# Kernel tuning notes

Measured on AMD Instinct MI355X. Metric: run time of the kernel, lower is better.

The kernel has to match this reference:

```python
import jax, jax.numpy as jnp
import numpy as np

NUM_OBJECTS = 6          # self.NUM_OBJECTS
SCORE_THRESH = 1e-4      # self.score_tresh
NMS_THRESHS = jnp.asarray(np.arange(0.001, 1.0, 0.1), dtype=jnp.float32)  # 10 thresholds
K_CAND = 1024            # fixed-shape cap on (proposal,class) candidates per image
CLASS_OFFSET = 4096.0    # > max image coord; batched_nms per-class offset trick


def _iou_matrix(b):
    # b: [K,4] xyxy -> [K,K] IoU
    x1, y1, x2, y2 = b[:, 0], b[:, 1], b[:, 2], b[:, 3]
    area = (x2 - x1) * (y2 - y1)
    iw = jnp.clip(jnp.minimum(x2[:, None], x2[None, :]) - jnp.maximum(x1[:, None], x1[None, :]), 0.0)
    ih = jnp.clip(jnp.minimum(y2[:, None], y2[None, :]) - jnp.maximum(y1[:, None], y1[None, :]), 0.0)
    inter = iw * ih
    union = area[:, None] + area[None, :] - inter
    return jnp.where(union > 0, inter / union, 0.0)


def _greedy_nms(iou, valid, thresh):
    # candidates are pre-sorted by descending score; sequential greedy suppression
    K = valid.shape[0]
    ar = jnp.arange(K)
    def body(i, keep):
        sup = keep[i] & (iou[i] > thresh) & (ar > i)
        return keep & ~sup
    return jax.lax.fori_loop(0, K, body, valid)


def _per_image(logits, boxes, feats, hw):
    # logits [N,81], boxes [N,80,4], feats [N,2048], hw [2] (h,w)
    C = boxes.shape[1]
    probs = jax.nn.softmax(logits, axis=-1)[:, :C]          # drop background class
    h = hw[0].astype(boxes.dtype)
    w = hw[1].astype(boxes.dtype)
    b = jnp.stack([jnp.clip(boxes[..., 0], 0.0, w),         # clip to image
                   jnp.clip(boxes[..., 1], 0.0, h),
                   jnp.clip(boxes[..., 2], 0.0, w),
                   jnp.clip(boxes[..., 3], 0.0, h)], axis=-1)
    scores = probs.reshape(-1)                              # [N*C]
    vals, idx = jax.lax.top_k(jnp.where(scores > SCORE_THRESH, scores, -1.0), K_CAND)
    cand_valid = vals > SCORE_THRESH
    cb = b.reshape(-1, 4)[idx]                              # [K,4]
    cls = (idx % C).astype(boxes.dtype)
    prop = idx // C                                         # proposal row index
    iou = _iou_matrix(cb + cls[:, None] * CLASS_OFFSET)     # per-class NMS via offsets
    keeps = jax.vmap(lambda t: _greedy_nms(iou, cand_valid, t))(NMS_THRESHS)  # [T,K]
    counts = keeps.sum(axis=1)
    # torch loop: break at first (smallest) thresh yielding len(ids)==6, i.e. >=6 kept
    ok = counts >= NUM_OBJECTS
    t_sel = jnp.where(jnp.any(ok), jnp.argmax(ok), NMS_THRESHS.shape[0] - 1)
    keep = keeps[t_sel]
    _, top = jax.lax.top_k(jnp.where(keep, vals, -jnp.inf), NUM_OBJECTS)
    ids = prop[top]                                         # [6]
    return feats[ids].T                                     # [2048, 6] (permute(1,0))


def _forward(cls_logits, boxes, feature_pooled, image_hw):
    return jax.vmap(_per_image)(cls_logits, boxes, feature_pooled, image_hw)  # [B,2048,6]


def setup_inputs() -> dict:
    key = jax.random.key(0)
    k1, k2, k3, k4, k5 = jax.random.split(key, 5)
    B, N, C, D = 8, 1000, 80, 2048
    cls_logits = jax.random.normal(k1, (B, N, C + 1), dtype=jnp.float32)
    ctr = jax.random.uniform(k2, (B, N, C, 2), minval=0.0, maxval=800.0)
    sz = jax.random.uniform(k3, (B, N, C, 2), minval=8.0, maxval=200.0)
    boxes = jnp.concatenate([ctr - sz * 0.5, ctr + sz * 0.5], axis=-1).astype(jnp.float32)
    feature_pooled = jax.random.normal(k4, (B, N, D), dtype=jnp.float32)
    image_hw = jax.random.randint(k5, (B, 2), 600, 800, dtype=jnp.int32)
    return {"cls_logits": cls_logits, "boxes": boxes,
            "feature_pooled": feature_pooled, "image_hw": image_hw}


def reference(cls_logits, boxes, feature_pooled, image_hw):
    return _forward(cls_logits, boxes, feature_pooled, image_hw)
```

## Files before the change

### kernel.cpp

```cpp
#include <hip/hip_runtime.h>
#include <cmath>
#include <cstdint>

#define NB 8
#define NPROP 1000
#define NCLS 80
#define NLOG 81
#define KCAND 1024
#define NTH 10
#define DFEAT 2048
#define NOBJ 6
#define NSCORE (NPROP*NCLS)
#define HBLK 8
#define HCHUNK (NSCORE/HBLK)
#define PCHUNK (NPROP/HBLK)

constexpr size_t OFF_SCORES = 0;
constexpr size_t SZ_SCORES  = (size_t)NB * NSCORE * 4;
constexpr size_t OFF_LISTA  = OFF_SCORES + SZ_SCORES;
constexpr size_t SZ_LISTA   = (size_t)NB * 20 * KCAND * 8;
constexpr size_t OFF_H1     = OFF_LISTA;
constexpr size_t OFF_H2     = OFF_H1 + (size_t)NB * HBLK * 2048 * 4;
constexpr size_t OFF_PIV    = OFF_H2 + (size_t)NB * HBLK * 2048 * 4;
constexpr size_t OFF_CBUF   = OFF_PIV + (size_t)NB * 8 * 4;
constexpr size_t OFF_CANDK  = OFF_LISTA + SZ_LISTA;
constexpr size_t SZ_CANDK   = (size_t)NB * KCAND * 8;
constexpr size_t OFF_CX1    = OFF_CANDK + SZ_CANDK;
constexpr size_t SZ_CARR    = (size_t)NB * KCAND * 4;
constexpr size_t OFF_CY1    = OFF_CX1 + SZ_CARR;
constexpr size_t OFF_CX2    = OFF_CY1 + SZ_CARR;
constexpr size_t OFF_CY2    = OFF_CX2 + SZ_CARR;
constexpr size_t OFF_CAREA  = OFF_CY2 + SZ_CARR;
constexpr size_t OFF_CPROP  = OFF_CAREA + SZ_CARR;
constexpr size_t OFF_VALIDW = OFF_CPROP + SZ_CARR;
constexpr size_t SZ_VALIDW  = (size_t)NB * 16 * 8;
constexpr size_t OFF_MASKS  = OFF_VALIDW + SZ_VALIDW;
constexpr size_t SZ_MASKS   = (size_t)NTH * NB * KCAND * 16 * 8;
constexpr size_t OFF_KEEPS  = OFF_MASKS + SZ_MASKS;
constexpr size_t SZ_KEEPS   = (size_t)NB * NTH * 16 * 8;
constexpr size_t OFF_COUNTS = OFF_KEEPS + SZ_KEEPS;
constexpr size_t SZ_COUNTS  = (size_t)NB * NTH * 4;
constexpr size_t OFF_CCLS   = OFF_COUNTS + SZ_COUNTS;
constexpr size_t SZ_CCLS    = (size_t)NB * KCAND * 4;

#define TSTRIDE ((size_t)NB * 16 * 1024)

__device__ __forceinline__ float nms_th(int t) {
    return (float)(0.001 + 0.1 * (double)t);
}

__device__ __forceinline__ unsigned score_vkey(float v) {
    float vv = (v > 1e-4f) ? v : -1.0f;
    unsigned bits = __float_as_uint(vv);
    unsigned u = (bits & 0x80000000u) ? ~bits : (bits | 0x80000000u);
    return ~u;
}

__global__ void k_memz(ulonglong2* __restrict__ p, int n) {
    int g = blockIdx.x * blockDim.x + threadIdx.x;
    if (g < n) p[g] = ulonglong2{0ULL, 0ULL};
}

__global__ __launch_bounds__(1024) void k_softhist(const float* __restrict__ logits,
                                                   float* __restrict__ scores,
                                                   unsigned* __restrict__ hist1) {
    __shared__ unsigned hh[2048];
    int img = blockIdx.x >> 3, blk = blockIdx.x & 7;
    int tid = threadIdx.x, wid = tid >> 6, lane = tid & 63;
    hh[tid] = 0; hh[tid + 1024] = 0;
    __syncthreads();
    for (int p = wid; p < PCHUNK; p += 16) {
        int prop = blk * PCHUNK + p;
        const float* L = logits + ((size_t)img * NPROP + prop) * NLOG;
        float l0 = L[lane];
        float l1 = (lane < 17) ? L[64 + lane] : -INFINITY;
        float m = fmaxf(l0, l1);
        #pragma unroll
        for (int o = 32; o > 0; o >>= 1) m = fmaxf(m, __shfl_xor(m, o, 64));
        float e0 = expf(l0 - m);
        float e1 = (lane < 17) ? expf(l1 - m) : 0.f;
        float s = e0 + e1;
        #pragma unroll
        for (int o = 32; o > 0; o >>= 1) s += __shfl_xor(s, o, 64);
        float* op = scores + ((size_t)img * NPROP + prop) * NCLS;
        float p0 = e0 / s;
        op[lane] = p0;
        atomicAdd(&hh[score_vkey(p0) >> 21], 1u);
        if (lane < 16) {
            float p1 = e1 / s;
            op[64 + lane] = p1;
            atomicAdd(&hh[score_vkey(p1) >> 21], 1u);
        }
    }
    __syncthreads();
    unsigned* outp = hist1 + ((size_t)img * HBLK + blk) * 2048;
    outp[tid] = hh[tid];
    outp[tid + 1024] = hh[tid + 1024];
}

__device__ __forceinline__ void pivot_scan(const unsigned* __restrict__ h8, unsigned K,
                                           int* __restrict__ out_b, int* __restrict__ out_rem) {
    __shared__ unsigned wsum[16];
    int tid = threadIdx.x;
    unsigned a = 0, b = 0;
    #pragma unroll
    for (int s = 0; s < HBLK; ++s) {
        a += h8[s * 2048 + 2 * tid];
        b += h8[s * 2048 + 2 * tid + 1];
    }
    unsigned p = a + b;
    unsigned x = p;
    #pragma unroll
    for (int d = 1; d < 64; d <<= 1) {
        unsigned y = __shfl_up(x, (unsigned)d, 64);
        if ((tid & 63) >= d) x += y;
    }
    if ((tid & 63) == 63) wsum[tid >> 6] = x;
    __syncthreads();
    if (tid < 16) {
        unsigned w = wsum[tid];
        #pragma unroll
        for (int d = 1; d < 16; d <<= 1) {
            unsigned y = __shfl_up(w, (unsigned)d, 64);
            if (tid >= d) w += y;
        }
        wsum[tid] = w;
    }
    __syncthreads();
    unsigned wex = (tid >= 64) ? wsum[(tid >> 6) - 1] : 0u;
    unsigned incl = x + wex;
    unsigned E = incl - p;
    if (E < K && E + a >= K)              { *out_b = 2 * tid;     *out_rem = (int)(K - E); }
    else if (E + a < K && E + a + b >= K) { *out_b = 2 * tid + 1; *out_rem = (int)(K - (E + a)); }
}

__global__ __launch_bounds__(1024) void k_hist2p(const float* __restrict__ scores,
                                                 const unsigned* __restrict__ hist1,
                                                 unsigned* __restrict__ hist2,
                                                 int* __restrict__ piv) {
    __shared__ unsigned hh[2048];
    __shared__ int sb, sr;
    int img = blockIdx.x >> 3, blk = blockIdx.x & 7;
    int tid = threadIdx.x;
    hh[tid] = 0; hh[tid + 1024] = 0;
    pivot_scan(hist1 + (size_t)img * HBLK * 2048, KCAND, &sb, &sr);
    __syncthreads();
    unsigned b1 = (unsigned)sb;
    const float* sc = scores + (size_t)img * NSCORE + (size_t)blk * HCHUNK;
    for (int e = tid; e < HCHUNK; e += 1024) {
        unsigned vk = score_vkey(sc[e]);
        if ((vk >> 21) == b1) atomicAdd(&hh[(vk >> 10) & 2047u], 1u);
    }
    __syncthreads();
    unsigned* outp = hist2 + ((size_t)img * HBLK + blk) * 2048;
    outp[tid] = hh[tid];
    outp[tid + 1024] = hh[tid + 1024];
    if (blk == 0 && tid == 0) {
        piv[img * 8 + 0] = sb;
        piv[img * 8 + 1] = sr;
        piv[img * 8 + 3] = 0;
    }
}

__global__ __launch_bounds__(1024) void k_gatherp(const float* __restrict__ scores,
                                                  const unsigned* __restrict__ hist2,
                                                  int* __restrict__ piv,
                                                  unsigned long long* __restrict__ cbuf) {
    __shared__ int sb2, sr2;
    __shared__ unsigned lcnt, gbase;
    int img = blockIdx.x >> 3, blk = blockIdx.x & 7;
    int tid = threadIdx.x;
    if (tid == 0) lcnt = 0;
    unsigned K2 = (unsigned)piv[img * 8 + 1];
    pivot_scan(hist2 + (size_t)img * HBLK * 2048, K2, &sb2, &sr2);
    __syncthreads();
    unsigned T22 = ((unsigned)piv[img * 8 + 0] << 11) | (unsigned)sb2;
    const float* sc = scores + (size_t)img * NSCORE + (size_t)blk * HCHUNK;
    unsigned long long sel[(HCHUNK + 1023) / 1024];
    int ns = 0;
    for (int e = tid; e < HCHUNK; e += 1024) {
        unsigned vk = score_vkey(sc[e]);
        if ((vk >> 10) <= T22)
            sel[ns++] = ((unsigned long long)vk << 32) | (unsigned)(blk * HCHUNK + e);
    }
    unsigned lp = atomicAdd(&lcnt, (unsigned)ns);
    __syncthreads();
    if (tid == 0) gbase = atomicAdd((unsigned*)&piv[img * 8 + 3], lcnt);
    __syncthreads();
    unsigned long long* ob = cbuf + (size_t)img * 2048;
    for (int i = 0; i < ns; ++i) {
        unsigned pos = gbase + lp + (unsigned)i;
        if (pos < 2048) ob[pos] = sel[i];
    }
}

__global__ __launch_bounds__(256) void k_rankcand(const unsigned long long* __restrict__ cbuf,
                                                  const int* __restrict__ piv,
                                                  const float* __restrict__ boxes,
                                                  const int* __restrict__ hw,
                                                  float* __restrict__ cx1, float* __restrict__ cy1,
                                                  float* __restrict__ cx2, float* __restrict__ cy2,
                                                  float* __restrict__ car, int* __restrict__ cprop,
                                                  int* __restrict__ ccls,
                                                  unsigned long long* __restrict__ validw) {
    __shared__ unsigned long long keys[2048];
    int img = blockIdx.x >> 3, sl = blockIdx.x & 7;
    int tid = threadIdx.x;
    int cnt = piv[img * 8 + 3]; if (cnt > 2048) cnt = 2048;
    const unsigned long long* ib = cbuf + (size_t)img * 2048;
    #pragma unroll
    for (int k = 0; k < 8; ++k) {
        int t = k * 256 + tid;
        keys[t] = (t < cnt) ? ib[t] : ~0ULL;
    }
    __syncthreads();
    unsigned long long a = keys[sl * 256 + tid];
    int r = 0;
    #pragma unroll 8
    for (int j = 0; j < cnt; ++j) r += (keys[j] < a) ? 1 : 0;
    if (r < KCAND) {
        unsigned u   = ~(unsigned)(a >> 32);
        unsigned idx = (unsigned)a;
        const unsigned uth = __float_as_uint(1e-4f) | 0x80000000u;
        bool valid = u > uth;
        int prop = (int)(idx / NCLS);
        int cls  = (int)(idx - (unsigned)prop * NCLS);
        const float4 bx = *(const float4*)(boxes + ((((size_t)img * NPROP + prop) * NCLS + cls) << 2));
        float h = (float)hw[img * 2 + 0];
        float w = (float)hw[img * 2 + 1];
        float x1 = fminf(fmaxf(bx.x, 0.f), w);
        float y1 = fminf(fmaxf(bx.y, 0.f), h);
        float x2 = fminf(fmaxf(bx.z, 0.f), w);
        float y2 = fminf(fmaxf(bx.w, 0.f), h);
        float offc = __fmul_rn((float)cls, 4096.0f);
        x1 = __fadd_rn(x1, offc); y1 = __fadd_rn(y1, offc);
        x2 = __fadd_rn(x2, offc); y2 = __fadd_rn(y2, offc);
        float area = __fmul_rn(__fsub_rn(x2, x1), __fsub_rn(y2, y1));
        int o = img * KCAND + r;
        cx1[o] = x1; cy1[o] = y1; cx2[o] = x2; cy2[o] = y2;
        car[o] = area; cprop[o] = prop; ccls[o] = cls;
        if (valid) atomicOr(&validw[img * 16 + (r >> 6)], 1ULL << (r & 63));
    }
}

__global__ void k_masks(const float* __restrict__ cx1, const float* __restrict__ cy1,
                        const float* __restrict__ cx2, const float* __restrict__ cy2,
                        const float* __restrict__ car, const int* __restrict__ ccls,
                        unsigned long long* __restrict__ masks) {
    int gw   = (blockIdx.x * blockDim.x + threadIdx.x) >> 6;
    int lane = threadIdx.x & 63;
    if (gw >= NB * KCAND) return;
    int bimg = gw >> 10;
    int i    = gw & (KCAND - 1);
    int cb   = bimg * KCAND;
    int   ci  = ccls[cb + i];
    float xi1 = cx1[cb + i], yi1 = cy1[cb + i];
    float xi2 = cx2[cb + i], yi2 = cy2[cb + i], ai = car[cb + i];
    int cmax = i >> 6;
    for (int c = 0; c <= cmax; ++c) {
        int j = c * 64 + lane;
        bool jlt = j < i;
        int cj = ccls[cb + j];
        if (__ballot(jlt && (cj == ci)) == 0ULL) continue;
        float xj1 = cx1[cb + j], yj1 = cy1[cb + j];
        float xj2 = cx2[cb + j], yj2 = cy2[cb + j], aj = car[cb + j];
        float iw = fmaxf(__fsub_rn(fminf(xi2, xj2), fmaxf(xi1, xj1)), 0.f);
        float ih = fmaxf(__fsub_rn(fminf(yi2, yj2), fmaxf(yi1, yj1)), 0.f);
        float inter = __fmul_rn(iw, ih);
        if (__ballot(jlt && (inter > 0.f)) == 0ULL) continue;
        float uni = __fsub_rn(__fadd_rn(ai, aj), inter);
        float iou = (uni > 0.f) ? __fdiv_rn(inter, uni) : 0.f;
        unsigned long long bl[NTH];
        #pragma unroll
        for (int t = 0; t < NTH; ++t) bl[t] = __ballot(jlt && (iou > nms_th(t)));
        unsigned long long myv = 0;
        #pragma unroll
        for (int t = 0; t < NTH; ++t) myv = (lane == t) ? bl[t] : myv;
        if (lane < NTH)
            masks[(size_t)lane * TSTRIDE + (((size_t)(bimg * 16 + c)) << 10) + i] = myv;
    }
}

__global__ __launch_bounds__(1024) void k_scan(const unsigned long long* __restrict__ masks,
                                               const unsigned long long* __restrict__ validw,
                                               unsigned long long* __restrict__ keeps,
                                               int* __restrict__ counts) {
    __shared__ unsigned long long kp[16];
    __shared__ int changed[2];
    int bt   = blockIdx.x;
    int bimg = bt / NTH, t = bt % NTH;
    int tid  = threadIdx.x;
    int w    = tid >> 6;
    int lane = tid & 63;
    const unsigned long long* mb = masks + (size_t)t * TSTRIDE + ((size_t)(bimg * 16) << 10);
    unsigned long long row[16];
    #pragma unroll
    for (int c = 0; c < 16; ++c)
        row[c] = (c <= w) ? mb[((size_t)c << 10) + tid] : 0ULL;
    unsigned long long vw = validw[bimg * 16 + w];
    bool valid = (vw >> lane) & 1ULL;
    if (tid < 16) kp[tid] = validw[bimg * 16 + tid];
    if (tid < 2) changed[tid] = 0;
    __syncthreads();
    for (int iter = 0; iter < KCAND + 2; ++iter) {
        unsigned long long s = 0;
        #pragma unroll
        for (int c = 0; c < 16; ++c) s |= row[c] & kp[c];
        bool nk = valid && (s == 0);
        unsigned long long bal = __ballot(nk);
        bool diff = (lane == 0) && (bal != kp[w]);
        __syncthreads();
        if (diff) { kp[w] = bal; changed[iter & 1] = 1; }
        if (tid == 0) changed[(iter + 1) & 1] = 0;
        __syncthreads();
        if (!changed[iter & 1]) break;
    }
    if (tid < 16) keeps[((size_t)bimg * NTH + t) * 16 + tid] = kp[tid];
    if (tid < 64) {
        int c = (lane < 16) ? __popcll(kp[lane]) : 0;
        #pragma unroll
        for (int o = 32; o > 0; o >>= 1) c += __shfl_xor(c, o, 64);
        if (lane == 0) counts[bimg * NTH + t] = c;
    }
}

__global__ __launch_bounds__(256) void k_selfeat(const int* __restrict__ counts,
                                                 const unsigned long long* __restrict__ keeps,
                                                 const int* __restrict__ cprop,
                                                 const float* __restrict__ feats,
                                                 float* __restrict__ outp) {
    __shared__ int scnt[NTH];
    __shared__ unsigned long long skw[16];
    __shared__ int stsel;
    __shared__ int sids[NOBJ];
    int img = blockIdx.x >> 3;
    int tid = threadIdx.x;
    if (tid < NTH) scnt[tid] = counts[img * NTH + tid];
    __syncthreads();
    if (tid == 0) {
        int tsel = NTH - 1;
        for (int t = 0; t < NTH; ++t) if (scnt[t] >= NOBJ) { tsel = t; break; }
        stsel = tsel;
    }
    __syncthreads();
    if (tid < 16) skw[tid] = keeps[((size_t)img * NTH + stsel) * 16 + tid];
    __syncthreads();
    if (tid == 0) {
        int got = 0;
        for (int k = 0; k < 16 && got < NOBJ; ++k) {
            unsigned long long x = skw[k];
            while (x && got < NOBJ) {
                int b = __builtin_ctzll(x);
                sids[got++] = cprop[img * KCAND + k * 64 + b];
                x &= x - 1;
            }
        }
        for (int k = 0; k < 16 && got < NOBJ; ++k) {
            unsigned long long x = ~skw[k];
            while (x && got < NOBJ) {
                int b = __builtin_ctzll(x);
                sids[got++] = cprop[img * KCAND + k * 64 + b];
                x &= x - 1;
            }
        }
    }
    __syncthreads();
    int d = (blockIdx.x & 7) * 256 + tid;
    const float* fb = feats + (size_t)img * NPROP * DFEAT;
    float* ob = outp + ((size_t)img * DFEAT + d) * NOBJ;
    #pragma unroll
    for (int s = 0; s < NOBJ; ++s)
        ob[s] = fb[(size_t)sids[s] * DFEAT + d];
}

extern "C" void kernel_launch(void* const* d_in, const int* in_sizes, int n_in,
                              void* d_out, int out_size, void* d_ws, size_t ws_size,
                              hipStream_t stream) {
    const float* logits = (const float*)d_in[0];
    const float* boxes  = (const float*)d_in[1];
    const float* feats  = (const float*)d_in[2];
    const int*   hw     = (const int*)d_in[3];
    float* outp = (float*)d_out;

    char* ws = (char*)d_ws;
    float*              scores = (float*)(ws + OFF_SCORES);
    unsigned*           hist1  = (unsigned*)(ws + OFF_H1);
    unsigned*           hist2  = (unsigned*)(ws + OFF_H2);
    int*                piv    = (int*)(ws + OFF_PIV);
    unsigned long long* cbuf   = (unsigned long long*)(ws + OFF_CBUF);
    float* cx1 = (float*)(ws + OFF_CX1);
    float* cy1 = (float*)(ws + OFF_CY1);
    float* cx2 = (float*)(ws + OFF_CX2);
    float* cy2 = (float*)(ws + OFF_CY2);
    float* car = (float*)(ws + OFF_CAREA);
    int*   cprop = (int*)(ws + OFF_CPROP);
    int*   ccls  = (int*)(ws + OFF_CCLS);
    unsigned long long* validw = (unsigned long long*)(ws + OFF_VALIDW);
    unsigned long long* masks  = (unsigned long long*)(ws + OFF_MASKS);
    unsigned long long* keeps  = (unsigned long long*)(ws + OFF_KEEPS);
    int* counts = (int*)(ws + OFF_COUNTS);

    const int mz_n = (int)((SZ_VALIDW + SZ_MASKS) / 16);
    k_memz<<<(mz_n + 255) / 256, 256, 0, stream>>>((ulonglong2*)(ws + OFF_VALIDW), mz_n);
    k_softhist<<<NB * HBLK, 1024, 0, stream>>>(logits, scores, hist1);
    k_hist2p<<<NB * HBLK, 1024, 0, stream>>>(scores, hist1, hist2, piv);
    k_gatherp<<<NB * HBLK, 1024, 0, stream>>>(scores, hist2, piv, cbuf);
    k_rankcand<<<NB * HBLK, 256, 0, stream>>>(cbuf, piv, boxes, hw,
                                              cx1, cy1, cx2, cy2, car, cprop, ccls, validw);
    k_masks<<<(NB * KCAND) / 4, 256, 0, stream>>>(cx1, cy1, cx2, cy2, car, ccls, masks);
    k_scan<<<NB * NTH, 1024, 0, stream>>>(masks, validw, keeps, counts);
    k_selfeat<<<NB * HBLK, 256, 0, stream>>>(counts, keeps, cprop, feats, outp);
}
```

Baseline: 169.4 us.

## Fuse the NMS pipeline into one cooperative kernel with grid syncs

Replaces the chain of eight kernel launches with a single cooperative mega-kernel of 256 blocks that separates the stages with grid.sync(). It also reorganises the work split: 32 blocks per image for softmax and histograms, and a warp-per-row mask build that skips chunks with no same-class or overlapping pairs. The aim is to remove launch gaps and tail idling between the small stages. In exchange, several stages now run on only a few blocks (rank on 32, scan on 80) while the rest wait at the barrier. If the cooperative launch fails, the old multi-kernel path still runs.

```diff
diff --git a/kernel.cpp b/kernel.cpp
--- a/kernel.cpp
+++ b/kernel.cpp
@@ -1,6 +1,9 @@
 #include <hip/hip_runtime.h>
+#include <hip/hip_cooperative_groups.h>
 #include <cmath>
 #include <cstdint>
+
+namespace cg = cooperative_groups;
 
 #define NB 8
 #define NPROP 1000
@@ -55,6 +58,332 @@
     unsigned u = (bits & 0x80000000u) ? ~bits : (bits | 0x80000000u);
     return ~u;
 }
+
+
+__device__ __forceinline__ void pivot512(const unsigned* __restrict__ h, unsigned K,
+                                         int* __restrict__ out_b, int* __restrict__ out_rem) {
+    __shared__ unsigned pwsum[8];
+    int tid = threadIdx.x, lane = tid & 63, wv = tid >> 6;
+    unsigned c0 = h[4 * tid + 0], c1 = h[4 * tid + 1];
+    unsigned c2 = h[4 * tid + 2], c3 = h[4 * tid + 3];
+    unsigned p = c0 + c1 + c2 + c3;
+    unsigned x = p;
+    #pragma unroll
+    for (int d = 1; d < 64; d <<= 1) {
+        unsigned y = __shfl_up(x, (unsigned)d, 64);
+        if (lane >= d) x += y;
+    }
+    if (lane == 63) pwsum[wv] = x;
+    __syncthreads();
+    if (tid < 8) {
+        unsigned w = pwsum[tid];
+        #pragma unroll
+        for (int d = 1; d < 8; d <<= 1) {
+            unsigned y = __shfl_up(w, (unsigned)d, 64);
+            if (tid >= d) w += y;
+        }
+        pwsum[tid] = w;
+    }
+    __syncthreads();
+    unsigned wex = wv ? pwsum[wv - 1] : 0u;
+    unsigned e0 = x + wex - p;
+    unsigned e1 = e0 + c0, e2 = e1 + c1, e3 = e2 + c2, e4 = e3 + c3;
+    if      (e0 < K && e1 >= K) { *out_b = 4 * tid + 0; *out_rem = (int)(K - e0); }
+    else if (e1 < K && e2 >= K) { *out_b = 4 * tid + 1; *out_rem = (int)(K - e1); }
+    else if (e2 < K && e3 >= K) { *out_b = 4 * tid + 2; *out_rem = (int)(K - e2); }
+    else if (e3 < K && e4 >= K) { *out_b = 4 * tid + 3; *out_rem = (int)(K - e3); }
+    __syncthreads();
+}
+
+__global__ __launch_bounds__(512, 2) void k_mega(
+        const float* __restrict__ logits, const float* __restrict__ boxes,
+        const float* __restrict__ feats, const int* __restrict__ hw,
+        float* __restrict__ outp,
+        float* __restrict__ scores, unsigned* __restrict__ gh1, unsigned* __restrict__ gh2,
+        int* __restrict__ cnt, unsigned long long* __restrict__ cbuf,
+        float* __restrict__ cx1, float* __restrict__ cy1,
+        float* __restrict__ cx2, float* __restrict__ cy2,
+        float* __restrict__ car, int* __restrict__ cprop, int* __restrict__ ccls,
+        unsigned long long* __restrict__ validw,
+        unsigned long long* __restrict__ masks,
+        unsigned long long* __restrict__ keeps, int* __restrict__ counts) {
+    cg::grid_group grid = cg::this_grid();
+    __shared__ union {
+        unsigned hist[2048];
+        unsigned long long keys[2048];
+        struct { int scnt[NTH]; unsigned long long skw[16]; int stsel; int sids[NOBJ]; } sel;
+    } sm;
+    __shared__ unsigned long long kp[16];
+    __shared__ int ichg[2];
+    __shared__ int sb1, sr1, sb2, sr2;
+    __shared__ unsigned lcnt, gbase;
+
+    const int blk = blockIdx.x;
+    const int tid = threadIdx.x;
+    const int wv  = tid >> 6, lane = tid & 63;
+    const int img = blk >> 5;
+    const int sl  = blk & 31;
+    const int pbeg = sl * 32;
+    const int pend = (pbeg + 32 < NPROP) ? (pbeg + 32) : NPROP;
+
+    {
+        int g = blk * 512 + tid;
+        if (g < NB * 2048) { gh1[g] = 0; gh2[g] = 0; }
+        if (g < NB) cnt[g] = 0;
+        if (g < NB * 16) validw[g] = 0ULL;
+    }
+    grid.sync();
+
+    {
+        #pragma unroll
+        for (int k = 0; k < 4; ++k) sm.hist[tid + k * 512] = 0;
+        __syncthreads();
+        for (int p = pbeg + wv; p < pend; p += 8) {
+            const float* L = logits + ((size_t)img * NPROP + p) * NLOG;
+            float l0 = L[lane];
+            float l1 = (lane < 17) ? L[64 + lane] : -INFINITY;
+            float m = fmaxf(l0, l1);
+            #pragma unroll
+            for (int o = 32; o > 0; o >>= 1) m = fmaxf(m, __shfl_xor(m, o, 64));
+            float e0 = expf(l0 - m);
+            float e1 = (lane < 17) ? expf(l1 - m) : 0.f;
+            float s = e0 + e1;
+            #pragma unroll
+            for (int o = 32; o > 0; o >>= 1) s += __shfl_xor(s, o, 64);
+            float* op = scores + ((size_t)img * NPROP + p) * NCLS;
+            float p0 = e0 / s;
+            op[lane] = p0;
+            atomicAdd(&sm.hist[score_vkey(p0) >> 21], 1u);
+            if (lane < 16) {
+                float p1 = e1 / s;
+                op[64 + lane] = p1;
+                atomicAdd(&sm.hist[score_vkey(p1) >> 21], 1u);
+            }
+        }
+        __syncthreads();
+        #pragma unroll
+        for (int k = 0; k < 4; ++k) {
+            unsigned v = sm.hist[tid + k * 512];
+            if (v) atomicAdd(&gh1[img * 2048 + tid + k * 512], v);
+        }
+    }
+    grid.sync();
+
+    {
+        pivot512(gh1 + (size_t)img * 2048, KCAND, &sb1, &sr1);
+        unsigned b1 = (unsigned)sb1;
+        #pragma unroll
+        for (int k = 0; k < 4; ++k) sm.hist[tid + k * 512] = 0;
+        __syncthreads();
+        const float* sc = scores + (size_t)img * NSCORE;
+        int ebeg = pbeg * NCLS, eend = pend * NCLS;
+        for (int e = ebeg + tid; e < eend; e += 512) {
+            unsigned vk = score_vkey(sc[e]);
+            if ((vk >> 21) == b1) atomicAdd(&sm.hist[(vk >> 10) & 2047u], 1u);
+        }
+        __syncthreads();
+        #pragma unroll
+        for (int k = 0; k < 4; ++k) {
+            unsigned v = sm.hist[tid + k * 512];
+            if (v) atomicAdd(&gh2[img * 2048 + tid + k * 512], v);
+        }
+    }
+    grid.sync();
+
+    {
+        pivot512(gh1 + (size_t)img * 2048, KCAND, &sb1, &sr1);
+        pivot512(gh2 + (size_t)img * 2048, (unsigned)sr1, &sb2, &sr2);
+        if (tid == 0) lcnt = 0;
+        __syncthreads();
+        unsigned T22 = ((unsigned)sb1 << 11) | (unsigned)sb2;
+        const float* sc = scores + (size_t)img * NSCORE;
+        int ebeg = pbeg * NCLS, eend = pend * NCLS;
+        unsigned long long selb[6];
+        int ns = 0;
+        for (int e = ebeg + tid; e < eend; e += 512) {
+            unsigned vk = score_vkey(sc[e]);
+            if ((vk >> 10) <= T22)
+                selb[ns++] = ((unsigned long long)vk << 32) | (unsigned)e;
+        }
+        unsigned lp = atomicAdd(&lcnt, (unsigned)ns);
+        __syncthreads();
+        if (tid == 0) gbase = atomicAdd((unsigned*)&cnt[img], lcnt);
+        __syncthreads();
+        unsigned long long* ob = cbuf + (size_t)img * 2048;
+        for (int i = 0; i < ns; ++i) {
+            unsigned pos = gbase + lp + (unsigned)i;
+            if (pos < 2048) ob[pos] = selb[i];
+        }
+    }
+    grid.sync();
+
+    if (sl < 4) {
+        int c = cnt[img]; if (c > 2048) c = 2048;
+        const unsigned long long* ib = cbuf + (size_t)img * 2048;
+        #pragma unroll
+        for (int k = 0; k < 4; ++k) {
+            int t = k * 512 + tid;
+            sm.keys[t] = (t < c) ? ib[t] : ~0ULL;
+        }
+        __syncthreads();
+        int my = sl * 512 + tid;
+        unsigned long long a = sm.keys[my];
+        int r = 0;
+        #pragma unroll 8
+        for (int j = 0; j < c; ++j) r += (sm.keys[j] < a) ? 1 : 0;
+        if (my < c && r < KCAND) {
+            unsigned u   = ~(unsigned)(a >> 32);
+            unsigned idx = (unsigned)a;
+            const unsigned uth = __float_as_uint(1e-4f) | 0x80000000u;
+            bool valid = u > uth;
+            int prop = (int)(idx / NCLS);
+            int cls  = (int)(idx - (unsigned)prop * NCLS);
+            const float4 bx = *(const float4*)(boxes + ((((size_t)img * NPROP + prop) * NCLS + cls) << 2));
+            float h = (float)hw[img * 2 + 0];
+            float w = (float)hw[img * 2 + 1];
+            float x1 = fminf(fmaxf(bx.x, 0.f), w);
+            float y1 = fminf(fmaxf(bx.y, 0.f), h);
+            float x2 = fminf(fmaxf(bx.z, 0.f), w);
+            float y2 = fminf(fmaxf(bx.w, 0.f), h);
+            float offc = __fmul_rn((float)cls, 4096.0f);
+            x1 = __fadd_rn(x1, offc); y1 = __fadd_rn(y1, offc);
+            x2 = __fadd_rn(x2, offc); y2 = __fadd_rn(y2, offc);
+            float area = __fmul_rn(__fsub_rn(x2, x1), __fsub_rn(y2, y1));
+            int o = img * KCAND + r;
+            cx1[o] = x1; cy1[o] = y1; cx2[o] = x2; cy2[o] = y2;
+            car[o] = area; cprop[o] = prop; ccls[o] = cls;
+            if (valid) atomicOr(&validw[img * 16 + (r >> 6)], 1ULL << (r & 63));
+        }
+    }
+    grid.sync();
+
+    {
+        int w = blk * 8 + wv;
+        for (int k = 0; k < 4; ++k) {
+            int rowg = w + 2048 * k;
+            int im = rowg >> 10;
+            int i  = rowg & 1023;
+            int cb = im * KCAND;
+            int   ci  = ccls[cb + i];
+            float xi1 = cx1[cb + i], yi1 = cy1[cb + i];
+            float xi2 = cx2[cb + i], yi2 = cy2[cb + i], ai = car[cb + i];
+            int cmax = i >> 6;
+            for (int c = 0; c <= cmax; ++c) {
+                int j = c * 64 + lane;
+                bool jlt = j < i;
+                unsigned long long bl[NTH];
+                #pragma unroll
+                for (int t = 0; t < NTH; ++t) bl[t] = 0ULL;
+                int cj = ccls[cb + j];
+                if (__ballot(jlt && (cj == ci)) != 0ULL) {
+                    float xj1 = cx1[cb + j], yj1 = cy1[cb + j];
+                    float xj2 = cx2[cb + j], yj2 = cy2[cb + j], aj = car[cb + j];
+                    float iw = fmaxf(__fsub_rn(fminf(xi2, xj2), fmaxf(xi1, xj1)), 0.f);
+                    float ih = fmaxf(__fsub_rn(fminf(yi2, yj2), fmaxf(yi1, yj1)), 0.f);
+                    float inter = __fmul_rn(iw, ih);
+                    if (__ballot(jlt && (inter > 0.f)) != 0ULL) {
+                        float uni = __fsub_rn(__fadd_rn(ai, aj), inter);
+                        float iou = (uni > 0.f) ? __fdiv_rn(inter, uni) : 0.f;
+                        #pragma unroll
+                        for (int t = 0; t < NTH; ++t) bl[t] = __ballot(jlt && (iou > nms_th(t)));
+                    }
+                }
+                unsigned long long myv = 0;
+                #pragma unroll
+                for (int t = 0; t < NTH; ++t) myv = (lane == t) ? bl[t] : myv;
+                if (lane < NTH)
+                    masks[(size_t)lane * TSTRIDE + (((size_t)(im * 16 + c)) << 10) + i] = myv;
+            }
+        }
+    }
+    grid.sync();
+
+    if (blk < NB * NTH) {
+        int im = blk / NTH, t = blk % NTH;
+        const unsigned long long* mb = masks + (size_t)t * TSTRIDE + ((size_t)(im * 16) << 10);
+        int iA = tid, iB = tid + 512;
+        int cA = iA >> 6;
+        int cB = iB >> 6;
+        unsigned long long rowA[8], rowB[16];
+        #pragma unroll
+        for (int c = 0; c < 8; ++c)  rowA[c] = (c <= cA) ? mb[((size_t)c << 10) + iA] : 0ULL;
+        #pragma unroll
+        for (int c = 0; c < 16; ++c) rowB[c] = (c <= cB) ? mb[((size_t)c << 10) + iB] : 0ULL;
+        bool vA = (validw[im * 16 + cA] >> (iA & 63)) & 1ULL;
+        bool vB = (validw[im * 16 + cB] >> (iB & 63)) & 1ULL;
+        if (tid < 16) kp[tid] = validw[im * 16 + tid];
+        if (tid < 2) ichg[tid] = 0;
+        __syncthreads();
+        for (int iter = 0; iter < KCAND + 2; ++iter) {
+            unsigned long long sA = 0, sB = 0;
+            #pragma unroll
+            for (int c = 0; c < 8; ++c)  sA |= rowA[c] & kp[c];
+            #pragma unroll
+            for (int c = 0; c < 16; ++c) sB |= rowB[c] & kp[c];
+            bool nkA = vA && (sA == 0);
+            bool nkB = vB && (sB == 0);
+            unsigned long long balA = __ballot(nkA);
+            unsigned long long balB = __ballot(nkB);
+            bool dA = (lane == 0) && (balA != kp[wv]);
+            bool dB = (lane == 0) && (balB != kp[wv + 8]);
+            __syncthreads();
+            if (dA) { kp[wv] = balA; ichg[iter & 1] = 1; }
+            if (dB) { kp[wv + 8] = balB; ichg[iter & 1] = 1; }
+            if (tid == 0) ichg[(iter + 1) & 1] = 0;
+            __syncthreads();
+            if (!ichg[iter & 1]) break;
+        }
+        if (tid < 16) keeps[((size_t)im * NTH + t) * 16 + tid] = kp[tid];
+        if (tid < 64) {
+            int c = (lane < 16) ? __popcll(kp[lane]) : 0;
+            #pragma unroll
+            for (int o = 32; o > 0; o >>= 1) c += __shfl_xor(c, o, 64);
+            if (lane == 0) counts[im * NTH + t] = c;
+        }
+    }
+    grid.sync();
+
+    if (blk < NB * 4) {
+        int im = blk >> 2;
+        if (tid < NTH) sm.sel.scnt[tid] = counts[im * NTH + tid];
+        __syncthreads();
+        if (tid == 0) {
+            int tsel = NTH - 1;
+            for (int t = 0; t < NTH; ++t) if (sm.sel.scnt[t] >= NOBJ) { tsel = t; break; }
+            sm.sel.stsel = tsel;
+        }
+        __syncthreads();
+        if (tid < 16) sm.sel.skw[tid] = keeps[((size_t)im * NTH + sm.sel.stsel) * 16 + tid];
+        __syncthreads();
+        if (tid == 0) {
+            int got = 0;
+            for (int k = 0; k < 16 && got < NOBJ; ++k) {
+                unsigned long long x = sm.sel.skw[k];
+                while (x && got < NOBJ) {
+                    int b = __builtin_ctzll(x);
+                    sm.sel.sids[got++] = cprop[im * KCAND + k * 64 + b];
+                    x &= x - 1;
+                }
+            }
+            for (int k = 0; k < 16 && got < NOBJ; ++k) {
+                unsigned long long x = ~sm.sel.skw[k];
+                while (x && got < NOBJ) {
+                    int b = __builtin_ctzll(x);
+                    sm.sel.sids[got++] = cprop[im * KCAND + k * 64 + b];
+                    x &= x - 1;
+                }
+            }
+        }
+        __syncthreads();
+        int d = (blk & 3) * 512 + tid;
+        const float* fb = feats + (size_t)im * NPROP * DFEAT;
+        float* ob = outp + ((size_t)im * DFEAT + d) * NOBJ;
+        #pragma unroll
+        for (int s = 0; s < NOBJ; ++s)
+            ob[s] = fb[(size_t)sm.sel.sids[s] * DFEAT + d];
+    }
+}
+
 
 __global__ void k_memz(ulonglong2* __restrict__ p, int n) {
     int g = blockIdx.x * blockDim.x + threadIdx.x;
@@ -400,6 +729,21 @@
     unsigned long long* keeps  = (unsigned long long*)(ws + OFF_KEEPS);
     int* counts = (int*)(ws + OFF_COUNTS);
 
+    {
+        unsigned* gh1 = hist1;
+        unsigned* gh2 = hist2;
+        int*      cnt = piv;
+        void* args[] = { (void*)&logits, (void*)&boxes, (void*)&feats, (void*)&hw, (void*)&outp,
+                         (void*)&scores, (void*)&gh1, (void*)&gh2, (void*)&cnt, (void*)&cbuf,
+                         (void*)&cx1, (void*)&cy1, (void*)&cx2, (void*)&cy2, (void*)&car,
+                         (void*)&cprop, (void*)&ccls, (void*)&validw,
+                         (void*)&masks, (void*)&keeps, (void*)&counts };
+        hipError_t e = hipLaunchCooperativeKernel((const void*)k_mega, dim3(256), dim3(512),
+                                                  args, 0, stream);
+        if (e == hipSuccess) return;
+        (void)hipGetLastError();
+    }
+
     const int mz_n = (int)((SZ_VALIDW + SZ_MASKS) / 16);
     k_memz<<<(mz_n + 255) / 256, 256, 0, stream>>>((ulonglong2*)(ws + OFF_VALIDW), mz_n);
     k_softhist<<<NB * HBLK, 1024, 0, stream>>>(logits, scores, hist1);
```

New measurement: 352.3 us. 108% more time.

## Replace global IoU masks and scan with per-class wavefront NMS

Applied to the files above, without the earlier changes.

Candidates are bucketed by class during ranking, and NMS for each (image, class) pair runs inside a single wavefront using shuffles and ballot-based fixed-point iteration across all thresholds. This removes the large mask buffer, its zeroing kernel, the mask kernel and the block-wide scan kernel, since the class offset means different classes never overlap. Zeroing of small buffers is folded into the gather kernel. The risk is the per-class cap of 64: a class with more than 64 candidates would silently drop entries.

```diff
diff --git a/kernel.cpp b/kernel.cpp
--- a/kernel.cpp
+++ b/kernel.cpp
@@ -14,6 +14,7 @@
 #define HBLK 8
 #define HCHUNK (NSCORE/HBLK)
 #define PCHUNK (NPROP/HBLK)
+#define CCAP 64
 
 constexpr size_t OFF_SCORES = 0;
 constexpr size_t SZ_SCORES  = (size_t)NB * NSCORE * 4;
@@ -34,16 +35,10 @@
 constexpr size_t OFF_CPROP  = OFF_CAREA + SZ_CARR;
 constexpr size_t OFF_VALIDW = OFF_CPROP + SZ_CARR;
 constexpr size_t SZ_VALIDW  = (size_t)NB * 16 * 8;
-constexpr size_t OFF_MASKS  = OFF_VALIDW + SZ_VALIDW;
-constexpr size_t SZ_MASKS   = (size_t)NTH * NB * KCAND * 16 * 8;
-constexpr size_t OFF_KEEPS  = OFF_MASKS + SZ_MASKS;
+constexpr size_t OFF_CCNT   = OFF_VALIDW + SZ_VALIDW;
+constexpr size_t OFF_CLIST  = OFF_CCNT + (size_t)NB * NCLS * 4;
+constexpr size_t OFF_KEEPS  = OFF_CLIST + (size_t)NB * NCLS * CCAP * 4;
 constexpr size_t SZ_KEEPS   = (size_t)NB * NTH * 16 * 8;
-constexpr size_t OFF_COUNTS = OFF_KEEPS + SZ_KEEPS;
-constexpr size_t SZ_COUNTS  = (size_t)NB * NTH * 4;
-constexpr size_t OFF_CCLS   = OFF_COUNTS + SZ_COUNTS;
-constexpr size_t SZ_CCLS    = (size_t)NB * KCAND * 4;
-
-#define TSTRIDE ((size_t)NB * 16 * 1024)
 
 __device__ __forceinline__ float nms_th(int t) {
     return (float)(0.001 + 0.1 * (double)t);
@@ -54,11 +49,6 @@
     unsigned bits = __float_as_uint(vv);
     unsigned u = (bits & 0x80000000u) ? ~bits : (bits | 0x80000000u);
     return ~u;
-}
-
-__global__ void k_memz(ulonglong2* __restrict__ p, int n) {
-    int g = blockIdx.x * blockDim.x + threadIdx.x;
-    if (g < n) p[g] = ulonglong2{0ULL, 0ULL};
 }
 
 __global__ __launch_bounds__(1024) void k_softhist(const float* __restrict__ logits,
@@ -165,11 +155,21 @@
 __global__ __launch_bounds__(1024) void k_gatherp(const float* __restrict__ scores,
                                                   const unsigned* __restrict__ hist2,
                                                   int* __restrict__ piv,
-                                                  unsigned long long* __restrict__ cbuf) {
+                                                  unsigned long long* __restrict__ cbuf,
+                                                  int* __restrict__ ccnt,
+                                                  unsigned long long* __restrict__ validw,
+                                                  unsigned long long* __restrict__ keeps) {
     __shared__ int sb2, sr2;
     __shared__ unsigned lcnt, gbase;
     int img = blockIdx.x >> 3, blk = blockIdx.x & 7;
     int tid = threadIdx.x;
+    if (blockIdx.x == 0) {
+        if (tid < NB * NCLS) ccnt[tid] = 0;
+        if (tid >= 640 && tid < 640 + NB * 16) validw[tid - 640] = 0ULL;
+    }
+    if (blockIdx.x == 1) {
+        for (int k = tid; k < NB * NTH * 16; k += 1024) keeps[k] = 0ULL;
+    }
     if (tid == 0) lcnt = 0;
     unsigned K2 = (unsigned)piv[img * 8 + 1];
     pivot_scan(hist2 + (size_t)img * HBLK * 2048, K2, &sb2, &sr2);
@@ -201,8 +201,8 @@
                                                   float* __restrict__ cx1, float* __restrict__ cy1,
                                                   float* __restrict__ cx2, float* __restrict__ cy2,
                                                   float* __restrict__ car, int* __restrict__ cprop,
-                                                  int* __restrict__ ccls,
-                                                  unsigned long long* __restrict__ validw) {
+                                                  unsigned long long* __restrict__ validw,
+                                                  int* __restrict__ ccnt, int* __restrict__ clist) {
     __shared__ unsigned long long keys[2048];
     int img = blockIdx.x >> 3, sl = blockIdx.x & 7;
     int tid = threadIdx.x;
@@ -218,7 +218,7 @@
     int r = 0;
     #pragma unroll 8
     for (int j = 0; j < cnt; ++j) r += (keys[j] < a) ? 1 : 0;
-    if (r < KCAND) {
+    if (sl * 256 + tid < cnt && r < KCAND) {
         unsigned u   = ~(unsigned)(a >> 32);
         unsigned idx = (unsigned)a;
         const unsigned uth = __float_as_uint(1e-4f) | 0x80000000u;
@@ -238,94 +238,83 @@
         float area = __fmul_rn(__fsub_rn(x2, x1), __fsub_rn(y2, y1));
         int o = img * KCAND + r;
         cx1[o] = x1; cy1[o] = y1; cx2[o] = x2; cy2[o] = y2;
-        car[o] = area; cprop[o] = prop; ccls[o] = cls;
+        car[o] = area; cprop[o] = prop;
         if (valid) atomicOr(&validw[img * 16 + (r >> 6)], 1ULL << (r & 63));
-    }
-}
-
-__global__ void k_masks(const float* __restrict__ cx1, const float* __restrict__ cy1,
-                        const float* __restrict__ cx2, const float* __restrict__ cy2,
-                        const float* __restrict__ car, const int* __restrict__ ccls,
-                        unsigned long long* __restrict__ masks) {
-    int gw   = (blockIdx.x * blockDim.x + threadIdx.x) >> 6;
+        int slot = atomicAdd(&ccnt[img * NCLS + cls], 1);
+        if (slot < CCAP) clist[(img * NCLS + cls) * CCAP + slot] = r;
+    }
+}
+
+__global__ __launch_bounds__(256) void k_cnms(const int* __restrict__ ccnt,
+                                              const int* __restrict__ clist,
+                                              const float* __restrict__ cx1,
+                                              const float* __restrict__ cy1,
+                                              const float* __restrict__ cx2,
+                                              const float* __restrict__ cy2,
+                                              const float* __restrict__ car,
+                                              const unsigned long long* __restrict__ validw,
+                                              unsigned long long* __restrict__ keeps) {
+    int gid  = blockIdx.x * 4 + (threadIdx.x >> 6);
     int lane = threadIdx.x & 63;
-    if (gw >= NB * KCAND) return;
-    int bimg = gw >> 10;
-    int i    = gw & (KCAND - 1);
-    int cb   = bimg * KCAND;
-    int   ci  = ccls[cb + i];
-    float xi1 = cx1[cb + i], yi1 = cy1[cb + i];
-    float xi2 = cx2[cb + i], yi2 = cy2[cb + i], ai = car[cb + i];
-    int cmax = i >> 6;
-    for (int c = 0; c <= cmax; ++c) {
-        int j = c * 64 + lane;
-        bool jlt = j < i;
-        int cj = ccls[cb + j];
-        if (__ballot(jlt && (cj == ci)) == 0ULL) continue;
-        float xj1 = cx1[cb + j], yj1 = cy1[cb + j];
-        float xj2 = cx2[cb + j], yj2 = cy2[cb + j], aj = car[cb + j];
-        float iw = fmaxf(__fsub_rn(fminf(xi2, xj2), fmaxf(xi1, xj1)), 0.f);
-        float ih = fmaxf(__fsub_rn(fminf(yi2, yj2), fmaxf(yi1, yj1)), 0.f);
+    if (gid >= NB * NCLS) return;
+    int img = gid / NCLS, cls = gid - img * NCLS;
+    int n = ccnt[img * NCLS + cls];
+    if (n > CCAP) n = CCAP;
+    if (n == 0) return;
+    int r = (lane < n) ? clist[(img * NCLS + cls) * CCAP + lane] : 0x7fffffff;
+    int pos = 0;
+    for (int j = 0; j < n; ++j) {
+        int rj = __shfl(r, j, 64);
+        pos += (rj < r) ? 1 : 0;
+    }
+    int srt = 0;
+    for (int j = 0; j < n; ++j) {
+        int pj = __shfl(pos, j, 64);
+        int rj = __shfl(r, j, 64);
+        if (pj == lane) srt = rj;
+    }
+    bool act = lane < n;
+    int base = img * KCAND;
+    float x1 = 0, y1 = 0, x2 = 0, y2 = 0, ar = 0;
+    bool val = false;
+    if (act) {
+        x1 = cx1[base + srt]; y1 = cy1[base + srt];
+        x2 = cx2[base + srt]; y2 = cy2[base + srt]; ar = car[base + srt];
+        val = (validw[img * 16 + (srt >> 6)] >> (srt & 63)) & 1ULL;
+    }
+    unsigned long long m[NTH];
+    #pragma unroll
+    for (int t = 0; t < NTH; ++t) m[t] = 0ULL;
+    for (int b = 0; b < n; ++b) {
+        float xj1 = __shfl(x1, b, 64), yj1 = __shfl(y1, b, 64);
+        float xj2 = __shfl(x2, b, 64), yj2 = __shfl(y2, b, 64);
+        float aj  = __shfl(ar, b, 64);
+        float iw = fmaxf(__fsub_rn(fminf(x2, xj2), fmaxf(x1, xj1)), 0.f);
+        float ih = fmaxf(__fsub_rn(fminf(y2, yj2), fmaxf(y1, yj1)), 0.f);
         float inter = __fmul_rn(iw, ih);
-        if (__ballot(jlt && (inter > 0.f)) == 0ULL) continue;
-        float uni = __fsub_rn(__fadd_rn(ai, aj), inter);
-        float iou = (uni > 0.f) ? __fdiv_rn(inter, uni) : 0.f;
-        unsigned long long bl[NTH];
-        #pragma unroll
-        for (int t = 0; t < NTH; ++t) bl[t] = __ballot(jlt && (iou > nms_th(t)));
-        unsigned long long myv = 0;
-        #pragma unroll
-        for (int t = 0; t < NTH; ++t) myv = (lane == t) ? bl[t] : myv;
-        if (lane < NTH)
-            masks[(size_t)lane * TSTRIDE + (((size_t)(bimg * 16 + c)) << 10) + i] = myv;
-    }
-}
-
-__global__ __launch_bounds__(1024) void k_scan(const unsigned long long* __restrict__ masks,
-                                               const unsigned long long* __restrict__ validw,
-                                               unsigned long long* __restrict__ keeps,
-                                               int* __restrict__ counts) {
-    __shared__ unsigned long long kp[16];
-    __shared__ int changed[2];
-    int bt   = blockIdx.x;
-    int bimg = bt / NTH, t = bt % NTH;
-    int tid  = threadIdx.x;
-    int w    = tid >> 6;
-    int lane = tid & 63;
-    const unsigned long long* mb = masks + (size_t)t * TSTRIDE + ((size_t)(bimg * 16) << 10);
-    unsigned long long row[16];
-    #pragma unroll
-    for (int c = 0; c < 16; ++c)
-        row[c] = (c <= w) ? mb[((size_t)c << 10) + tid] : 0ULL;
-    unsigned long long vw = validw[bimg * 16 + w];
-    bool valid = (vw >> lane) & 1ULL;
-    if (tid < 16) kp[tid] = validw[bimg * 16 + tid];
-    if (tid < 2) changed[tid] = 0;
-    __syncthreads();
-    for (int iter = 0; iter < KCAND + 2; ++iter) {
-        unsigned long long s = 0;
-        #pragma unroll
-        for (int c = 0; c < 16; ++c) s |= row[c] & kp[c];
-        bool nk = valid && (s == 0);
-        unsigned long long bal = __ballot(nk);
-        bool diff = (lane == 0) && (bal != kp[w]);
-        __syncthreads();
-        if (diff) { kp[w] = bal; changed[iter & 1] = 1; }
-        if (tid == 0) changed[(iter + 1) & 1] = 0;
-        __syncthreads();
-        if (!changed[iter & 1]) break;
-    }
-    if (tid < 16) keeps[((size_t)bimg * NTH + t) * 16 + tid] = kp[tid];
-    if (tid < 64) {
-        int c = (lane < 16) ? __popcll(kp[lane]) : 0;
-        #pragma unroll
-        for (int o = 32; o > 0; o >>= 1) c += __shfl_xor(c, o, 64);
-        if (lane == 0) counts[bimg * NTH + t] = c;
-    }
-}
-
-__global__ __launch_bounds__(256) void k_selfeat(const int* __restrict__ counts,
-                                                 const unsigned long long* __restrict__ keeps,
+        float uni   = __fsub_rn(__fadd_rn(ar, aj), inter);
+        float iou   = (uni > 0.f) ? __fdiv_rn(inter, uni) : 0.f;
+        if (act && b < lane) {
+            #pragma unroll
+            for (int t = 0; t < NTH; ++t)
+                if (iou > nms_th(t)) m[t] |= 1ULL << b;
+        }
+    }
+    unsigned long long vmask = __ballot(act && val);
+    for (int t = 0; t < NTH; ++t) {
+        unsigned long long keep = vmask;
+        for (int it = 0; it <= n; ++it) {
+            bool nk = act && val && ((m[t] & keep) == 0ULL);
+            unsigned long long nb = __ballot(nk);
+            if (nb == keep) break;
+            keep = nb;
+        }
+        if (act && ((keep >> lane) & 1ULL))
+            atomicOr(&keeps[((size_t)img * NTH + t) * 16 + (srt >> 6)], 1ULL << (srt & 63));
+    }
+}
+
+__global__ __launch_bounds__(256) void k_selfeat(const unsigned long long* __restrict__ keeps,
                                                  const int* __restrict__ cprop,
                                                  const float* __restrict__ feats,
                                                  float* __restrict__ outp) {
@@ -335,7 +324,13 @@
     __shared__ int sids[NOBJ];
     int img = blockIdx.x >> 3;
     int tid = threadIdx.x;
-    if (tid < NTH) scnt[tid] = counts[img * NTH + tid];
+    if (tid < NTH) scnt[tid] = 0;
+    __syncthreads();
+    if (tid < NTH * 16) {
+        unsigned long long w = keeps[(size_t)img * NTH * 16 + tid];
+        int pc = __popcll(w);
+        if (pc) atomicAdd(&scnt[tid >> 4], pc);
+    }
     __syncthreads();
     if (tid == 0) {
         int tsel = NTH - 1;
@@ -394,20 +389,18 @@
     float* cy2 = (float*)(ws + OFF_CY2);
     float* car = (float*)(ws + OFF_CAREA);
     int*   cprop = (int*)(ws + OFF_CPROP);
-    int*   ccls  = (int*)(ws + OFF_CCLS);
     unsigned long long* validw = (unsigned long long*)(ws + OFF_VALIDW);
-    unsigned long long* masks  = (unsigned long long*)(ws + OFF_MASKS);
+    int*   ccnt  = (int*)(ws + OFF_CCNT);
+    int*   clist = (int*)(ws + OFF_CLIST);
     unsigned long long* keeps  = (unsigned long long*)(ws + OFF_KEEPS);
-    int* counts = (int*)(ws + OFF_COUNTS);
-
-    const int mz_n = (int)((SZ_VALIDW + SZ_MASKS) / 16);
-    k_memz<<<(mz_n + 255) / 256, 256, 0, stream>>>((ulonglong2*)(ws + OFF_VALIDW), mz_n);
+
     k_softhist<<<NB * HBLK, 1024, 0, stream>>>(logits, scores, hist1);
     k_hist2p<<<NB * HBLK, 1024, 0, stream>>>(scores, hist1, hist2, piv);
-    k_gatherp<<<NB * HBLK, 1024, 0, stream>>>(scores, hist2, piv, cbuf);
+    k_gatherp<<<NB * HBLK, 1024, 0, stream>>>(scores, hist2, piv, cbuf, ccnt, validw, keeps);
     k_rankcand<<<NB * HBLK, 256, 0, stream>>>(cbuf, piv, boxes, hw,
-                                              cx1, cy1, cx2, cy2, car, cprop, ccls, validw);
-    k_masks<<<(NB * KCAND) / 4, 256, 0, stream>>>(cx1, cy1, cx2, cy2, car, ccls, masks);
-    k_scan<<<NB * NTH, 1024, 0, stream>>>(masks, validw, keeps, counts);
-    k_selfeat<<<NB * HBLK, 256, 0, stream>>>(counts, keeps, cprop, feats, outp);
-}
+                                              cx1, cy1, cx2, cy2, car, cprop,
+                                              validw, ccnt, clist);
+    k_cnms<<<(NB * NCLS + 3) / 4, 256, 0, stream>>>(ccnt, clist, cx1, cy1, cx2, cy2,
+                                                    car, validw, keeps);
+    k_selfeat<<<NB * HBLK, 256, 0, stream>>>(keeps, cprop, feats, outp);
+}
```

New measurement: 163.6 us. -3.4%, faster.
